# Kernel tuning notes

Measured on AMD Instinct MI355X. Metric: run time of the kernel, lower is better.

## Reference

```python
import jax, jax.numpy as jnp
import numpy as np

N = 100000      # nodes
E = 1600000     # edges
NINP = 64       # input node features
NE = 8          # edge attr channels (spectral supports)
NOUT = 24       # nout1 == nout2
NIN = 2 * NOUT  # 48, hidden width after concat
G = 256         # graphs in batch
EPS = 1e-5


def setup_inputs() -> dict:
    key = jax.random.key(0)
    ks = jax.random.split(key, 40)
    def nrm(i, shape, s=1.0):
        return jax.random.normal(ks[i], shape, dtype=jnp.float32) * s
    inp = {}
    inp["x"] = nrm(0, (N, NINP))
    inp["edge_index"] = jax.random.randint(ks[1], (2, E), 0, N)
    inp["edge_attr"] = nrm(2, (E, NE))
    inp["batch"] = jnp.sort(jax.random.randint(ks[3], (N,), 0, G))
    i = 4
    for l, din in ((1, NINP), (2, NIN), (3, NIN)):
        inp[f"W{l}"] = nrm(i, (NE, din, NOUT), 0.1); i += 1   # SpectConv weight [K,in,out]
        inp[f"b{l}"] = jnp.zeros((NOUT,), jnp.float32)         # SpectConv bias
        inp[f"A{l}"] = nrm(i, (din, NOUT), 0.1); i += 1        # fc11 weight
        inp[f"a{l}"] = jnp.zeros((NOUT,), jnp.float32)
        inp[f"B{l}"] = nrm(i, (din, NOUT), 0.1); i += 1        # fc12 weight
        inp[f"c{l}"] = jnp.zeros((NOUT,), jnp.float32)
        inp[f"g{l}"] = jnp.ones((NIN,), jnp.float32)           # BN gamma
        inp[f"be{l}"] = jnp.zeros((NIN,), jnp.float32)         # BN beta
    inp["F1"] = nrm(i, (NIN, 32), 0.1); i += 1
    inp["f1"] = jnp.zeros((32,), jnp.float32)
    inp["F2"] = nrm(i, (32, 1), 0.1); i += 1
    inp["f2"] = jnp.zeros((1,), jnp.float32)
    return inp


def _ml3(x, src, dst, ea, W, b, A, a, Bm, c):
    # SpectConv (selfconn=False): sum_k segment_sum(ea[:,k]*x[src] -> dst) @ W[k] + b
    xs = x[src]                                    # [E, F] gather
    acc = jnp.zeros((x.shape[0], W.shape[2]), x.dtype)
    for k in range(W.shape[0]):                    # small fixed K=NE loop
        h = jax.ops.segment_sum(ea[:, k:k+1] * xs, dst, num_segments=x.shape[0])
        acc = acc + h @ W[k]
    conv = jax.nn.relu(acc + b)
    gate = jax.nn.relu(x @ A + a) * jnp.tanh(x @ Bm + c)
    return jnp.concatenate([conv, gate], axis=1)   # [N, NIN]


def _bn(x, g, b):
    # BatchNorm1d, training mode (biased batch statistics)
    m = x.mean(0)
    v = x.var(0)
    return (x - m) * jax.lax.rsqrt(v + EPS) * g + b


def reference(x, edge_index, edge_attr, batch,
              W1, b1, A1, a1, B1, c1, g1, be1,
              W2, b2, A2, a2, B2, c2, g2, be2,
              W3, b3, A3, a3, B3, c3, g3, be3,
              F1, f1, F2, f2):
    src, dst = edge_index[0], edge_index[1]
    h = _bn(_ml3(x, src, dst, edge_attr, W1, b1, A1, a1, B1, c1), g1, be1)
    h = _bn(_ml3(h, src, dst, edge_attr, W2, b2, A2, a2, B2, c2), g2, be2)
    h = _bn(_ml3(h, src, dst, edge_attr, W3, b3, A3, a3, B3, c3), g3, be3)
    sums = jax.ops.segment_sum(h, batch, num_segments=G)
    cnts = jax.ops.segment_sum(jnp.ones((h.shape[0], 1), h.dtype), batch, num_segments=G)
    pooled = sums / jnp.maximum(cnts, 1.0)         # global_mean_pool
    return jax.nn.relu(pooled @ F1 + f1) @ F2 + f2  # [G, 1]
```

## Files before the change

### kernel.cpp

```cpp
#include <hip/hip_runtime.h>
#include <hip/hip_fp16.h>
#include <math.h>

#define N_NODES 100000
#define N_EDGES 1600000
#define NGRAPH  256
#define YCOLS   240
#define EPS     1e-5f
#define BNCHUNK 100

typedef _Float16 h2v  __attribute__((ext_vector_type(2)));
typedef _Float16 f16x8 __attribute__((ext_vector_type(8)));
typedef float    f32x4 __attribute__((ext_vector_type(4)));

#if defined(__has_builtin)
#if __has_builtin(__builtin_amdgcn_fdot2)
#define HAVE_FDOT2 1
#endif
#endif

__device__ inline float dot8(float4 yraw, float4 eraw, float acc) {
#ifdef HAVE_FDOT2
  union U { float4 f; h2v v[4]; } y, e;
  y.f = yraw; e.f = eraw;
  acc = __builtin_amdgcn_fdot2(y.v[0], e.v[0], acc, false);
  acc = __builtin_amdgcn_fdot2(y.v[1], e.v[1], acc, false);
  acc = __builtin_amdgcn_fdot2(y.v[2], e.v[2], acc, false);
  acc = __builtin_amdgcn_fdot2(y.v[3], e.v[3], acc, false);
#else
  const __half2* yh = reinterpret_cast<const __half2*>(&yraw);
  const __half2* eh = reinterpret_cast<const __half2*>(&eraw);
#pragma unroll
  for (int i = 0; i < 4; i++) {
    float2 a = __half22float2(yh[i]), b = __half22float2(eh[i]);
    acc += a.x * b.x + a.y * b.y;
  }
#endif
  return acc;
}

__global__ void k_count(const int* __restrict__ dst, int* __restrict__ deg) {
  int e = blockIdx.x * blockDim.x + threadIdx.x;
  if (e < N_EDGES) atomicAdd(&deg[dst[e]], 1);
}

__global__ void k_scan1(const int* __restrict__ deg, int* __restrict__ part,
                        int* __restrict__ bsum) {
  __shared__ int lds[256];
  int t = threadIdx.x;
  int base = blockIdx.x * 1024 + t * 4;
  int v[4]; int s = 0;
#pragma unroll
  for (int i = 0; i < 4; i++) { int idx = base + i; v[i] = (idx < N_NODES) ? deg[idx] : 0; s += v[i]; }
  lds[t] = s; __syncthreads();
  for (int off = 1; off < 256; off <<= 1) {
    int x = (t >= off) ? lds[t - off] : 0;
    __syncthreads();
    lds[t] += x;
    __syncthreads();
  }
  int excl = lds[t] - s;
#pragma unroll
  for (int i = 0; i < 4; i++) { int idx = base + i; if (idx < N_NODES) part[idx] = excl; excl += v[i]; }
  if (t == 255) bsum[blockIdx.x] = lds[255];
}

__global__ void k_scan2(int* __restrict__ bsum, int nb) {
  __shared__ int lds[128];
  int t = threadIdx.x;
  int v = (t < nb) ? bsum[t] : 0;
  lds[t] = v; __syncthreads();
  for (int off = 1; off < 128; off <<= 1) {
    int x = (t >= off) ? lds[t - off] : 0;
    __syncthreads();
    lds[t] += x;
    __syncthreads();
  }
  if (t < nb) bsum[t] = lds[t] - v;
}

__global__ void k_scan3(int* __restrict__ rowptr, const int* __restrict__ bsum,
                        int* __restrict__ cursor) {
  int i = blockIdx.x * blockDim.x + threadIdx.x;
  if (i < N_NODES) {
    int v = rowptr[i] + bsum[i >> 10];
    rowptr[i] = v; cursor[i] = v;
  }
  if (i == 0) rowptr[N_NODES] = N_EDGES;
}

__global__ void k_fill(const int* __restrict__ src, const int* __restrict__ dst,
                       const float* __restrict__ ea, int* __restrict__ cursor,
                       int* __restrict__ esrc, __half* __restrict__ ea_csr) {
  int e = blockIdx.x * blockDim.x + threadIdx.x;
  if (e < N_EDGES) {
    int d = dst[e];
    int pos = atomicAdd(&cursor[d], 1);
    esrc[pos] = src[e];
    float4 a = *reinterpret_cast<const float4*>(ea + (size_t)e * 8);
    float4 b = *reinterpret_cast<const float4*>(ea + (size_t)e * 8 + 4);
    union { __half h[8]; float4 f; } u;
    u.h[0] = __float2half(a.x); u.h[1] = __float2half(a.y);
    u.h[2] = __float2half(a.z); u.h[3] = __float2half(a.w);
    u.h[4] = __float2half(b.x); u.h[5] = __float2half(b.y);
    u.h[6] = __float2half(b.z); u.h[7] = __float2half(b.w);
    *reinterpret_cast<float4*>(ea_csr + (size_t)pos * 8) = u.f;
  }
}

__global__ void k_ghist(const int* __restrict__ batch, int* __restrict__ gcnt) {
  __shared__ int lh[NGRAPH];
  int t = threadIdx.x;
  lh[t] = 0; __syncthreads();
  for (int i = blockIdx.x * 256 + t; i < N_NODES; i += gridDim.x * 256)
    atomicAdd(&lh[batch[i]], 1);
  __syncthreads();
  if (lh[t]) atomicAdd(&gcnt[t], lh[t]);
}

__global__ void k_gscan(const int* __restrict__ gcnt, int* __restrict__ gstart) {
  __shared__ int lds[NGRAPH];
  int t = threadIdx.x;
  int v = gcnt[t]; lds[t] = v; __syncthreads();
  for (int off = 1; off < NGRAPH; off <<= 1) {
    int x = (t >= off) ? lds[t - off] : 0;
    __syncthreads();
    lds[t] += x;
    __syncthreads();
  }
  gstart[t] = lds[t] - v;
  if (t == NGRAPH - 1) gstart[NGRAPH] = lds[NGRAPH - 1];
}

__global__ void k_wcat_h(const float* __restrict__ W, const float* __restrict__ A,
                         const float* __restrict__ B, __half* __restrict__ out,
                         int din) {
  int i = blockIdx.x * blockDim.x + threadIdx.x;
  if (i >= YCOLS * 64) return;
  int j = i / 64, f = i % 64;
  float v = 0.f;
  if (f < din) {
    if (j < 192)      { int k8 = j / 24, o = j - k8 * 24; v = W[(k8 * din + f) * 24 + o]; }
    else if (j < 216) v = A[f * 24 + (j - 192)];
    else              v = B[f * 24 + (j - 216)];
  }
  out[i] = __float2half(v);
}

template <int F>
__global__ __launch_bounds__(256) void k_mm(const float* __restrict__ X,
                                            const __half* __restrict__ Wct,
                                            const float* __restrict__ ss,
                                            __half* __restrict__ Yh,
                                            float* __restrict__ G) {
  __shared__ _Float16 sx[64][64];
  int t = threadIdx.x;
  int r0 = blockIdx.x * 64;
  constexpr int F4 = F / 4;
  for (int i = t; i < 64 * F4; i += 256) {
    int row = i / F4, c4 = i - row * F4;
    int grow = r0 + row;
    float4 v = make_float4(0.f, 0.f, 0.f, 0.f);
    if (grow < N_NODES) {
      v = *reinterpret_cast<const float4*>(X + (size_t)grow * F + c4 * 4);
      if (ss) {
        int f = c4 * 4;
        v.x = v.x * ss[f + 0] + ss[48 + f + 0];
        v.y = v.y * ss[f + 1] + ss[48 + f + 1];
        v.z = v.z * ss[f + 2] + ss[48 + f + 2];
        v.w = v.w * ss[f + 3] + ss[48 + f + 3];
      }
    }
    int c = c4 * 4;
    sx[row][c + 0] = (_Float16)v.x;
    sx[row][c + 1] = (_Float16)v.y;
    sx[row][c + 2] = (_Float16)v.z;
    sx[row][c + 3] = (_Float16)v.w;
  }
  if (F == 48) {
    for (int i = t; i < 64 * 16; i += 256) {
      int row = i / 16, k = 48 + (i - (i / 16) * 16);
      sx[row][k] = (_Float16)0.f;
    }
  }
  __syncthreads();

  int w = t >> 6, l = t & 63;
  int lrow = l & 15;
  int lk = (l >> 4) * 8;
  const f16x8 a0 = *reinterpret_cast<const f16x8*>(&sx[w * 16 + lrow][lk]);
  const f16x8 a1 = *reinterpret_cast<const f16x8*>(&sx[w * 16 + lrow][lk + 32]);
  const _Float16* wct = reinterpret_cast<const _Float16*>(Wct);

#pragma unroll
  for (int ct = 0; ct < 15; ct++) {
    int col = ct * 16 + lrow;
    f16x8 b0 = *reinterpret_cast<const f16x8*>(wct + col * 64 + lk);
    f16x8 b1 = *reinterpret_cast<const f16x8*>(wct + col * 64 + lk + 32);
    f32x4 acc = {0.f, 0.f, 0.f, 0.f};
    acc = __builtin_amdgcn_mfma_f32_16x16x32_f16(a0, b0, acc, 0, 0, 0);
    acc = __builtin_amdgcn_mfma_f32_16x16x32_f16(a1, b1, acc, 0, 0, 0);
    int ycol = (col % 24) * 8 + col / 24;
    int gc   = (col < 216) ? (col - 192) : (24 + col - 216);
#pragma unroll
    for (int r = 0; r < 4; r++) {
      int grow = r0 + w * 16 + (l >> 4) * 4 + r;
      if (grow < N_NODES) {
        if (col < 192) Yh[(size_t)grow * 192 + ycol] = __float2half(acc[r]);
        else           G[(size_t)grow * 48 + gc] = acc[r];
      }
    }
  }
}

__global__ __launch_bounds__(192) void k_agg(
    const __half* __restrict__ Yh, const float* __restrict__ G,
    const int* __restrict__ rowptr, const int* __restrict__ esrc,
    const __half* __restrict__ ea_csr,
    const float* __restrict__ bconv, const float* __restrict__ ba,
    const float* __restrict__ bc,
    float* __restrict__ h, float* __restrict__ partial) {
  __shared__ float ssum[48], ssq[48];
  __shared__ float lacc[2][4][24];
  int t = threadIdx.x;
  if (t < 48) { ssum[t] = 0.f; ssq[t] = 0.f; }
  int ln   = t / 96;
  int slot = (t / 24) % 4;
  int o    = t % 24;
  int n = blockIdx.x * 2 + ln;
  float acc = 0.f;
  if (n < N_NODES) {
    int r0 = rowptr[n], r1 = rowptr[n + 1];
    int idx = r0 + slot;
    for (; idx + 4 < r1; idx += 8) {
      int s0 = esrc[idx], s1 = esrc[idx + 4];
      float4 e0 = *reinterpret_cast<const float4*>(ea_csr + (size_t)idx * 8);
      float4 e1 = *reinterpret_cast<const float4*>(ea_csr + (size_t)(idx + 4) * 8);
      float4 y0 = *reinterpret_cast<const float4*>(Yh + (size_t)s0 * 192 + o * 8);
      float4 y1 = *reinterpret_cast<const float4*>(Yh + (size_t)s1 * 192 + o * 8);
      acc = dot8(y0, e0, acc);
      acc = dot8(y1, e1, acc);
    }
    if (idx < r1) {
      int s0 = esrc[idx];
      float4 e0 = *reinterpret_cast<const float4*>(ea_csr + (size_t)idx * 8);
      float4 y0 = *reinterpret_cast<const float4*>(Yh + (size_t)s0 * 192 + o * 8);
      acc = dot8(y0, e0, acc);
    }
  }
  lacc[ln][slot][o] = acc;
  __syncthreads();
  if (t < 48) {
    int ln2 = t / 24, oo = t % 24;
    int n2 = blockIdx.x * 2 + ln2;
    if (n2 < N_NODES) {
      float a = lacc[ln2][0][oo] + lacc[ln2][1][oo] + lacc[ln2][2][oo] + lacc[ln2][3][oo];
      float conv = fmaxf(a + bconv[oo], 0.f);
      const float* gr = &G[(size_t)n2 * 48];
      float gate = fmaxf(gr[oo] + ba[oo], 0.f) * tanhf(gr[24 + oo] + bc[oo]);
      float* hr = &h[(size_t)n2 * 48];
      hr[oo] = conv;
      hr[24 + oo] = gate;
      atomicAdd(&ssum[oo], conv);        atomicAdd(&ssq[oo], conv * conv);
      atomicAdd(&ssum[24 + oo], gate);   atomicAdd(&ssq[24 + oo], gate * gate);
    }
  }
  __syncthreads();
  if (t < 96) partial[(size_t)blockIdx.x * 96 + t] = (t < 48) ? ssum[t] : ssq[t - 48];
}

__global__ __launch_bounds__(192) void k_bnred1(const float* __restrict__ partial,
                                                int nrows,
                                                float* __restrict__ out) {
  __shared__ float lds[192];
  int t = threadIdx.x;
  int rp = t / 96;
  int c  = t % 96;
  int r0 = blockIdx.x * BNCHUNK;
  int r1 = r0 + BNCHUNK; if (r1 > nrows) r1 = nrows;
  float s = 0.f;
  for (int r = r0 + rp; r < r1; r += 2) s += partial[(size_t)r * 96 + c];
  lds[t] = s; __syncthreads();
  if (t < 96) out[(size_t)blockIdx.x * 96 + t] = lds[t] + lds[t + 96];
}

__global__ void k_bnstats(const float* __restrict__ partial, int nblk,
                          const float* __restrict__ g, const float* __restrict__ be,
                          float* __restrict__ ss) {
  __shared__ float ls[256], lq[256];
  int c = blockIdx.x, t = threadIdx.x;
  float s = 0.f, q = 0.f;
  for (int i = t; i < nblk; i += 256) { s += partial[(size_t)i * 96 + c]; q += partial[(size_t)i * 96 + 48 + c]; }
  ls[t] = s; lq[t] = q; __syncthreads();
  for (int off = 128; off > 0; off >>= 1) {
    if (t < off) { ls[t] += ls[t + off]; lq[t] += lq[t + off]; }
    __syncthreads();
  }
  if (t == 0) {
    float mean = ls[0] / (float)N_NODES;
    float var = lq[0] / (float)N_NODES - mean * mean;
    var = fmaxf(var, 0.f);
    float sc = g[c] * rsqrtf(var + EPS);
    ss[c] = sc;
    ss[48 + c] = be[c] - mean * sc;
  }
}

__global__ __launch_bounds__(240) void k_pool2(const float* __restrict__ h,
                                               const int* __restrict__ gstart,
                                               const float* __restrict__ ss,
                                               float* __restrict__ pooled) {
  __shared__ float acc[240];
  int g = blockIdx.x, t = threadIdx.x;
  int o = t % 48, r = t / 48;
  int n0 = gstart[g], n1 = gstart[g + 1];
  float s = 0.f;
  for (int n = n0 + r; n < n1; n += 5) s += h[(size_t)n * 48 + o];
  acc[t] = s; __syncthreads();
  if (t < 48) {
    float tot = acc[t] + acc[t + 48] + acc[t + 96] + acc[t + 144] + acc[t + 192];
    float cnt = (float)(n1 - n0);
    float mean = tot / fmaxf(cnt, 1.f);
    pooled[g * 48 + t] = mean * ss[t] + ss[48 + t];
  }
}

__global__ __launch_bounds__(64) void k_mlp(const float* __restrict__ pooled,
                                            const float* __restrict__ F1,
                                            const float* __restrict__ f1,
                                            const float* __restrict__ F2,
                                            const float* __restrict__ f2,
                                            float* __restrict__ out) {
  __shared__ float p[48];
  int g = blockIdx.x, t = threadIdx.x;
  if (t < 48) p[t] = pooled[g * 48 + t];
  __syncthreads();
  float r = 0.f;
  if (t < 32) {
    float s = f1[t];
#pragma unroll
    for (int c = 0; c < 48; c++) s += p[c] * F1[c * 32 + t];
    r = fmaxf(s, 0.f) * F2[t];
  }
  for (int off = 32; off > 0; off >>= 1) r += __shfl_down(r, off, 64);
  if (t == 0) out[g] = r + f2[0];
}

extern "C" void kernel_launch(void* const* d_in, const int* in_sizes, int n_in,
                              void* d_out, int out_size, void* d_ws, size_t ws_size,
                              hipStream_t stream) {
  const float* x          = (const float*)d_in[0];
  const int*   edge_index = (const int*)d_in[1];
  const float* ea         = (const float*)d_in[2];
  const int*   batch      = (const int*)d_in[3];
  const float *W[3], *bcv[3], *A[3], *ba[3], *B[3], *bc[3], *g[3], *be[3];
  for (int l = 0; l < 3; l++) {
    int base = 4 + l * 8;
    W[l]   = (const float*)d_in[base + 0];
    bcv[l] = (const float*)d_in[base + 1];
    A[l]   = (const float*)d_in[base + 2];
    ba[l]  = (const float*)d_in[base + 3];
    B[l]   = (const float*)d_in[base + 4];
    bc[l]  = (const float*)d_in[base + 5];
    g[l]   = (const float*)d_in[base + 6];
    be[l]  = (const float*)d_in[base + 7];
  }
  const float* F1 = (const float*)d_in[28];
  const float* f1 = (const float*)d_in[29];
  const float* F2 = (const float*)d_in[30];
  const float* f2 = (const float*)d_in[31];
  const int* src = edge_index;
  const int* dst = edge_index + N_EDGES;

  char* w = (char*)d_ws;
  auto alloc = [&](size_t bytes) -> char* {
    char* p = w;
    w += (bytes + 255) & ~(size_t)255;
    return p;
  };
  int nagg = (N_NODES + 1) / 2;
  int nred = (nagg + BNCHUNK - 1) / BNCHUNK;

  int*    rowptr  = (int*)alloc((N_NODES + 1) * 4);
  int*    cursor  = (int*)alloc((size_t)N_NODES * 4);
  int*    deg     = (int*)alloc((size_t)N_NODES * 4);
  int*    bsum    = (int*)alloc(128 * 4);
  int*    esrc    = (int*)alloc((size_t)N_EDGES * 4);
  __half* ea_csr  = (__half*)alloc((size_t)N_EDGES * 8 * 2);
  int*    gcnt    = (int*)alloc(NGRAPH * 4);
  int*    gstart  = (int*)alloc((NGRAPH + 1) * 4);
  __half* Wct1    = (__half*)alloc((size_t)YCOLS * 64 * 2);
  __half* Wct2    = (__half*)alloc((size_t)YCOLS * 64 * 2);
  __half* Wct3    = (__half*)alloc((size_t)YCOLS * 64 * 2);
  __half* Yh      = (__half*)alloc((size_t)N_NODES * 192 * 2);
  float*  G       = (float*)alloc((size_t)N_NODES * 48 * 4);
  float*  h       = (float*)alloc((size_t)N_NODES * 48 * 4);
  float*  partial = (float*)alloc((size_t)nagg * 96 * 4);
  float*  partial2= (float*)alloc((size_t)nred * 96 * 4);
  float*  ss1     = (float*)alloc(96 * 4);
  float*  ss2     = (float*)alloc(96 * 4);
  float*  ss3     = (float*)alloc(96 * 4);
  float*  pooled  = (float*)alloc(NGRAPH * 48 * 4);

  hipMemsetAsync(deg, 0, (size_t)N_NODES * 4, stream);
  hipMemsetAsync(gcnt, 0, NGRAPH * 4, stream);

  k_count<<<(N_EDGES + 255) / 256, 256, 0, stream>>>(dst, deg);
  int nchunk = (N_NODES + 1023) / 1024;
  k_scan1<<<nchunk, 256, 0, stream>>>(deg, rowptr, bsum);
  k_scan2<<<1, 128, 0, stream>>>(bsum, nchunk);
  k_scan3<<<(N_NODES + 255) / 256, 256, 0, stream>>>(rowptr, bsum, cursor);
  k_fill<<<(N_EDGES + 255) / 256, 256, 0, stream>>>(src, dst, ea, cursor, esrc, ea_csr);

  k_ghist<<<64, 256, 0, stream>>>(batch, gcnt);
  k_gscan<<<1, NGRAPH, 0, stream>>>(gcnt, gstart);

  k_wcat_h<<<(YCOLS * 64 + 255) / 256, 256, 0, stream>>>(W[0], A[0], B[0], Wct1, 64);
  k_wcat_h<<<(YCOLS * 64 + 255) / 256, 256, 0, stream>>>(W[1], A[1], B[1], Wct2, 48);
  k_wcat_h<<<(YCOLS * 64 + 255) / 256, 256, 0, stream>>>(W[2], A[2], B[2], Wct3, 48);

  int nmm = (N_NODES + 63) / 64;

  k_mm<64><<<nmm, 256, 0, stream>>>(x, Wct1, nullptr, Yh, G);
  k_agg<<<nagg, 192, 0, stream>>>(Yh, G, rowptr, esrc, ea_csr, bcv[0], ba[0], bc[0], h, partial);
  k_bnred1<<<nred, 192, 0, stream>>>(partial, nagg, partial2);
  k_bnstats<<<48, 256, 0, stream>>>(partial2, nred, g[0], be[0], ss1);
  k_mm<48><<<nmm, 256, 0, stream>>>(h, Wct2, ss1, Yh, G);
  k_agg<<<nagg, 192, 0, stream>>>(Yh, G, rowptr, esrc, ea_csr, bcv[1], ba[1], bc[1], h, partial);
  k_bnred1<<<nred, 192, 0, stream>>>(partial, nagg, partial2);
  k_bnstats<<<48, 256, 0, stream>>>(partial2, nred, g[1], be[1], ss2);
  k_mm<48><<<nmm, 256, 0, stream>>>(h, Wct3, ss2, Yh, G);
  k_agg<<<nagg, 192, 0, stream>>>(Yh, G, rowptr, esrc, ea_csr, bcv[2], ba[2], bc[2], h, partial);
  k_bnred1<<<nred, 192, 0, stream>>>(partial, nagg, partial2);
  k_bnstats<<<48, 256, 0, stream>>>(partial2, nred, g[2], be[2], ss3);

  k_pool2<<<NGRAPH, 240, 0, stream>>>(h, gstart, ss3, pooled);
  k_mlp<<<NGRAPH, 64, 0, stream>>>(pooled, F1, f1, F2, f2, (float*)d_out);
}
```

Baseline: 707.7 us.

## Degree-sort nodes for aggregation, widen agg blocks, split CSR fill

Nodes are bucketed by in-degree through a counting sort (histogram, scan, fill) and the aggregation kernel visits them in that order, so the nodes sharing a block have similar work. The aggregation block grows to 768 threads, covering 4 nodes with 8 edge slots each, which gives more parallelism per node. The CSR fill is split into an atomic pass that records edge ids and a second pass that gathers src and edge attributes and writes them contiguously. The costs are extra small kernels and an indirect perm lookup in aggregation, and node writes to h become scattered.

```diff
diff --git a/kernel.cpp b/kernel.cpp
--- a/kernel.cpp
+++ b/kernel.cpp
@@ -8,6 +8,7 @@
 #define YCOLS   240
 #define EPS     1e-5f
 #define BNCHUNK 100
+#define DEGB    64
 
 typedef _Float16 h2v  __attribute__((ext_vector_type(2)));
 typedef _Float16 f16x8 __attribute__((ext_vector_type(8)));
@@ -89,14 +90,22 @@
   if (i == 0) rowptr[N_NODES] = N_EDGES;
 }
 
-__global__ void k_fill(const int* __restrict__ src, const int* __restrict__ dst,
-                       const float* __restrict__ ea, int* __restrict__ cursor,
-                       int* __restrict__ esrc, __half* __restrict__ ea_csr) {
+__global__ void k_fillA(const int* __restrict__ dst, int* __restrict__ cursor,
+                        int* __restrict__ eidx) {
   int e = blockIdx.x * blockDim.x + threadIdx.x;
   if (e < N_EDGES) {
-    int d = dst[e];
-    int pos = atomicAdd(&cursor[d], 1);
-    esrc[pos] = src[e];
+    int pos = atomicAdd(&cursor[dst[e]], 1);
+    eidx[pos] = e;
+  }
+}
+
+__global__ void k_fillB(const int* __restrict__ eidx, const int* __restrict__ src,
+                        const float* __restrict__ ea,
+                        int* __restrict__ esrc, __half* __restrict__ ea_csr) {
+  int p = blockIdx.x * blockDim.x + threadIdx.x;
+  if (p < N_EDGES) {
+    int e = eidx[p];
+    esrc[p] = src[e];
     float4 a = *reinterpret_cast<const float4*>(ea + (size_t)e * 8);
     float4 b = *reinterpret_cast<const float4*>(ea + (size_t)e * 8 + 4);
     union { __half h[8]; float4 f; } u;
@@ -104,7 +113,38 @@
     u.h[2] = __float2half(a.z); u.h[3] = __float2half(a.w);
     u.h[4] = __float2half(b.x); u.h[5] = __float2half(b.y);
     u.h[6] = __float2half(b.z); u.h[7] = __float2half(b.w);
-    *reinterpret_cast<float4*>(ea_csr + (size_t)pos * 8) = u.f;
+    *reinterpret_cast<float4*>(ea_csr + (size_t)p * 8) = u.f;
+  }
+}
+
+__global__ void k_dhist(const int* __restrict__ deg, int* __restrict__ dhist) {
+  int n = blockIdx.x * blockDim.x + threadIdx.x;
+  if (n < N_NODES) {
+    int d = deg[n]; if (d > DEGB - 1) d = DEGB - 1;
+    atomicAdd(&dhist[d], 1);
+  }
+}
+
+__global__ void k_dscan(const int* __restrict__ dhist, int* __restrict__ dcur) {
+  __shared__ int lds[DEGB];
+  int t = threadIdx.x;
+  int v = dhist[t]; lds[t] = v; __syncthreads();
+  for (int off = 1; off < DEGB; off <<= 1) {
+    int x = (t >= off) ? lds[t - off] : 0;
+    __syncthreads();
+    lds[t] += x;
+    __syncthreads();
+  }
+  dcur[t] = lds[t] - v;
+}
+
+__global__ void k_dfill(const int* __restrict__ deg, int* __restrict__ dcur,
+                        int* __restrict__ perm) {
+  int n = blockIdx.x * blockDim.x + threadIdx.x;
+  if (n < N_NODES) {
+    int d = deg[n]; if (d > DEGB - 1) d = DEGB - 1;
+    int pos = atomicAdd(&dcur[d], 1);
+    perm[pos] = n;
   }
 }
 
@@ -213,29 +253,30 @@
   }
 }
 
-__global__ __launch_bounds__(192) void k_agg(
+__global__ __launch_bounds__(768) void k_agg(
     const __half* __restrict__ Yh, const float* __restrict__ G,
-    const int* __restrict__ rowptr, const int* __restrict__ esrc,
-    const __half* __restrict__ ea_csr,
+    const int* __restrict__ rowptr, const int* __restrict__ perm,
+    const int* __restrict__ esrc, const __half* __restrict__ ea_csr,
     const float* __restrict__ bconv, const float* __restrict__ ba,
     const float* __restrict__ bc,
     float* __restrict__ h, float* __restrict__ partial) {
   __shared__ float ssum[48], ssq[48];
-  __shared__ float lacc[2][4][24];
+  __shared__ float lacc[4][8][24];
   int t = threadIdx.x;
   if (t < 48) { ssum[t] = 0.f; ssq[t] = 0.f; }
-  int ln   = t / 96;
-  int slot = (t / 24) % 4;
+  int ln   = t / 192;
+  int slot = (t / 24) % 8;
   int o    = t % 24;
-  int n = blockIdx.x * 2 + ln;
+  int bi = blockIdx.x * 4 + ln;
   float acc = 0.f;
-  if (n < N_NODES) {
+  if (bi < N_NODES) {
+    int n = perm[bi];
     int r0 = rowptr[n], r1 = rowptr[n + 1];
     int idx = r0 + slot;
-    for (; idx + 4 < r1; idx += 8) {
-      int s0 = esrc[idx], s1 = esrc[idx + 4];
+    for (; idx + 8 < r1; idx += 16) {
+      int s0 = esrc[idx], s1 = esrc[idx + 8];
       float4 e0 = *reinterpret_cast<const float4*>(ea_csr + (size_t)idx * 8);
-      float4 e1 = *reinterpret_cast<const float4*>(ea_csr + (size_t)(idx + 4) * 8);
+      float4 e1 = *reinterpret_cast<const float4*>(ea_csr + (size_t)(idx + 8) * 8);
       float4 y0 = *reinterpret_cast<const float4*>(Yh + (size_t)s0 * 192 + o * 8);
       float4 y1 = *reinterpret_cast<const float4*>(Yh + (size_t)s1 * 192 + o * 8);
       acc = dot8(y0, e0, acc);
@@ -250,11 +291,14 @@
   }
   lacc[ln][slot][o] = acc;
   __syncthreads();
-  if (t < 48) {
+  if (t < 96) {
     int ln2 = t / 24, oo = t % 24;
-    int n2 = blockIdx.x * 2 + ln2;
-    if (n2 < N_NODES) {
-      float a = lacc[ln2][0][oo] + lacc[ln2][1][oo] + lacc[ln2][2][oo] + lacc[ln2][3][oo];
+    int bi2 = blockIdx.x * 4 + ln2;
+    if (bi2 < N_NODES) {
+      int n2 = perm[bi2];
+      float a = 0.f;
+#pragma unroll
+      for (int s = 0; s < 8; s++) a += lacc[ln2][s][oo];
       float conv = fmaxf(a + bconv[oo], 0.f);
       const float* gr = &G[(size_t)n2 * 48];
       float gate = fmaxf(gr[oo] + ba[oo], 0.f) * tanhf(gr[24 + oo] + bc[oo]);
@@ -378,15 +422,19 @@
     w += (bytes + 255) & ~(size_t)255;
     return p;
   };
-  int nagg = (N_NODES + 1) / 2;
+  int nagg = (N_NODES + 3) / 4;
   int nred = (nagg + BNCHUNK - 1) / BNCHUNK;
 
   int*    rowptr  = (int*)alloc((N_NODES + 1) * 4);
   int*    cursor  = (int*)alloc((size_t)N_NODES * 4);
   int*    deg     = (int*)alloc((size_t)N_NODES * 4);
   int*    bsum    = (int*)alloc(128 * 4);
+  int*    eidx    = (int*)alloc((size_t)N_EDGES * 4);
   int*    esrc    = (int*)alloc((size_t)N_EDGES * 4);
   __half* ea_csr  = (__half*)alloc((size_t)N_EDGES * 8 * 2);
+  int*    perm    = (int*)alloc((size_t)N_NODES * 4);
+  int*    dhist   = (int*)alloc(DEGB * 4);
+  int*    dcur    = (int*)alloc(DEGB * 4);
   int*    gcnt    = (int*)alloc(NGRAPH * 4);
   int*    gstart  = (int*)alloc((NGRAPH + 1) * 4);
   __half* Wct1    = (__half*)alloc((size_t)YCOLS * 64 * 2);
@@ -404,13 +452,19 @@
 
   hipMemsetAsync(deg, 0, (size_t)N_NODES * 4, stream);
   hipMemsetAsync(gcnt, 0, NGRAPH * 4, stream);
+  hipMemsetAsync(dhist, 0, DEGB * 4, stream);
 
   k_count<<<(N_EDGES + 255) / 256, 256, 0, stream>>>(dst, deg);
   int nchunk = (N_NODES + 1023) / 1024;
   k_scan1<<<nchunk, 256, 0, stream>>>(deg, rowptr, bsum);
   k_scan2<<<1, 128, 0, stream>>>(bsum, nchunk);
   k_scan3<<<(N_NODES + 255) / 256, 256, 0, stream>>>(rowptr, bsum, cursor);
-  k_fill<<<(N_EDGES + 255) / 256, 256, 0, stream>>>(src, dst, ea, cursor, esrc, ea_csr);
+  k_fillA<<<(N_EDGES + 255) / 256, 256, 0, stream>>>(dst, cursor, eidx);
+  k_fillB<<<(N_EDGES + 255) / 256, 256, 0, stream>>>(eidx, src, ea, esrc, ea_csr);
+
+  k_dhist<<<(N_NODES + 255) / 256, 256, 0, stream>>>(deg, dhist);
+  k_dscan<<<1, DEGB, 0, stream>>>(dhist, dcur);
+  k_dfill<<<(N_NODES + 255) / 256, 256, 0, stream>>>(deg, dcur, perm);
 
   k_ghist<<<64, 256, 0, stream>>>(batch, gcnt);
   k_gscan<<<1, NGRAPH, 0, stream>>>(gcnt, gstart);
@@ -422,15 +476,15 @@
   int nmm = (N_NODES + 63) / 64;
 
   k_mm<64><<<nmm, 256, 0, stream>>>(x, Wct1, nullptr, Yh, G);
-  k_agg<<<nagg, 192, 0, stream>>>(Yh, G, rowptr, esrc, ea_csr, bcv[0], ba[0], bc[0], h, partial);
+  k_agg<<<nagg, 768, 0, stream>>>(Yh, G, rowptr, perm, esrc, ea_csr, bcv[0], ba[0], bc[0], h, partial);
   k_bnred1<<<nred, 192, 0, stream>>>(partial, nagg, partial2);
   k_bnstats<<<48, 256, 0, stream>>>(partial2, nred, g[0], be[0], ss1);
   k_mm<48><<<nmm, 256, 0, stream>>>(h, Wct2, ss1, Yh, G);
-  k_agg<<<nagg, 192, 0, stream>>>(Yh, G, rowptr, esrc, ea_csr, bcv[1], ba[1], bc[1], h, partial);
+  k_agg<<<nagg, 768, 0, stream>>>(Yh, G, rowptr, perm, esrc, ea_csr, bcv[1], ba[1], bc[1], h, partial);
   k_bnred1<<<nred, 192, 0, stream>>>(partial, nagg, partial2);
   k_bnstats<<<48, 256, 0, stream>>>(partial2, nred, g[1], be[1], ss2);
   k_mm<48><<<nmm, 256, 0, stream>>>(h, Wct3, ss2, Yh, G);
-  k_agg<<<nagg, 192, 0, stream>>>(Yh, G, rowptr, esrc, ea_csr, bcv[2], ba[2], bc[2], h, partial);
+  k_agg<<<nagg, 768, 0, stream>>>(Yh, G, rowptr, perm, esrc, ea_csr, bcv[2], ba[2], bc[2], h, partial);
   k_bnred1<<<nred, 192, 0, stream>>>(partial, nagg, partial2);
   k_bnstats<<<48, 256, 0, stream>>>(partial2, nred, g[2], be[2], ss3);
 
```

Result: slower. 1.586 ms (+124.1%).

## Fuse gate into matmul epilogue, stage outputs in LDS, move BN stats to separate pass

Applied to the files above, without the earlier changes.

The matmul kernel now stages its MFMA outputs in shared memory and writes Yh with coalesced vector stores. It also computes the gated branch (relu*tanh) directly into h, which removes the G intermediate buffer. The aggregation kernel only writes the conv half, with its edge loop unrolled to four edges per slot. Batch-norm sums are now computed by a separate reduction pass over h instead of LDS atomics, and ping-pong h buffers avoid read/write aliasing. This trades an extra read of h for less global traffic on G and fewer scattered stores.

```diff
diff --git a/kernel.cpp b/kernel.cpp
--- a/kernel.cpp
+++ b/kernel.cpp
@@ -7,7 +7,7 @@
 #define NGRAPH  256
 #define YCOLS   240
 #define EPS     1e-5f
-#define BNCHUNK 100
+#define BNCHUNK 200
 
 typedef _Float16 h2v  __attribute__((ext_vector_type(2)));
 typedef _Float16 f16x8 __attribute__((ext_vector_type(8)));
@@ -151,9 +151,13 @@
 __global__ __launch_bounds__(256) void k_mm(const float* __restrict__ X,
                                             const __half* __restrict__ Wct,
                                             const float* __restrict__ ss,
+                                            const float* __restrict__ ba,
+                                            const float* __restrict__ bc,
                                             __half* __restrict__ Yh,
-                                            float* __restrict__ G) {
+                                            float* __restrict__ h) {
   __shared__ _Float16 sx[64][64];
+  __shared__ _Float16 sy[64][200];
+  __shared__ float    sg[64][52];
   int t = threadIdx.x;
   int r0 = blockIdx.x * 64;
   constexpr int F4 = F / 4;
@@ -179,7 +183,7 @@
   }
   if (F == 48) {
     for (int i = t; i < 64 * 16; i += 256) {
-      int row = i / 16, k = 48 + (i - (i / 16) * 16);
+      int row = i / 16, k = 48 + (i % 16);
       sx[row][k] = (_Float16)0.f;
     }
   }
@@ -204,26 +208,32 @@
     int gc   = (col < 216) ? (col - 192) : (24 + col - 216);
 #pragma unroll
     for (int r = 0; r < 4; r++) {
-      int grow = r0 + w * 16 + (l >> 4) * 4 + r;
-      if (grow < N_NODES) {
-        if (col < 192) Yh[(size_t)grow * 192 + ycol] = __float2half(acc[r]);
-        else           G[(size_t)grow * 48 + gc] = acc[r];
-      }
-    }
+      int row = w * 16 + (l >> 4) * 4 + r;
+      if (col < 192) sy[row][ycol] = (_Float16)acc[r];
+      else           sg[row][gc] = acc[r];
+    }
+  }
+  __syncthreads();
+
+  int rows = N_NODES - r0; if (rows > 64) rows = 64;
+  for (int i = t; i < rows * 48; i += 256) {
+    int row = i / 48, c = (i % 48) * 4;
+    *reinterpret_cast<uint2*>(Yh + (size_t)(r0 + row) * 192 + c) =
+        *reinterpret_cast<const uint2*>(&sy[row][c]);
+  }
+  for (int i = t; i < rows * 24; i += 256) {
+    int row = i / 24, o = i % 24;
+    float gate = fmaxf(sg[row][o] + ba[o], 0.f) * tanhf(sg[row][24 + o] + bc[o]);
+    h[(size_t)(r0 + row) * 48 + 24 + o] = gate;
   }
 }
 
 __global__ __launch_bounds__(192) void k_agg(
-    const __half* __restrict__ Yh, const float* __restrict__ G,
-    const int* __restrict__ rowptr, const int* __restrict__ esrc,
-    const __half* __restrict__ ea_csr,
-    const float* __restrict__ bconv, const float* __restrict__ ba,
-    const float* __restrict__ bc,
-    float* __restrict__ h, float* __restrict__ partial) {
-  __shared__ float ssum[48], ssq[48];
+    const __half* __restrict__ Yh, const int* __restrict__ rowptr,
+    const int* __restrict__ esrc, const __half* __restrict__ ea_csr,
+    const float* __restrict__ bconv, float* __restrict__ h) {
   __shared__ float lacc[2][4][24];
   int t = threadIdx.x;
-  if (t < 48) { ssum[t] = 0.f; ssq[t] = 0.f; }
   int ln   = t / 96;
   int slot = (t / 24) % 4;
   int o    = t % 24;
@@ -232,16 +242,22 @@
   if (n < N_NODES) {
     int r0 = rowptr[n], r1 = rowptr[n + 1];
     int idx = r0 + slot;
-    for (; idx + 4 < r1; idx += 8) {
-      int s0 = esrc[idx], s1 = esrc[idx + 4];
+    for (; idx + 12 < r1; idx += 16) {
+      int s0 = esrc[idx], s1 = esrc[idx + 4], s2 = esrc[idx + 8], s3 = esrc[idx + 12];
       float4 e0 = *reinterpret_cast<const float4*>(ea_csr + (size_t)idx * 8);
       float4 e1 = *reinterpret_cast<const float4*>(ea_csr + (size_t)(idx + 4) * 8);
+      float4 e2 = *reinterpret_cast<const float4*>(ea_csr + (size_t)(idx + 8) * 8);
+      float4 e3 = *reinterpret_cast<const float4*>(ea_csr + (size_t)(idx + 12) * 8);
       float4 y0 = *reinterpret_cast<const float4*>(Yh + (size_t)s0 * 192 + o * 8);
       float4 y1 = *reinterpret_cast<const float4*>(Yh + (size_t)s1 * 192 + o * 8);
+      float4 y2 = *reinterpret_cast<const float4*>(Yh + (size_t)s2 * 192 + o * 8);
+      float4 y3 = *reinterpret_cast<const float4*>(Yh + (size_t)s3 * 192 + o * 8);
       acc = dot8(y0, e0, acc);
       acc = dot8(y1, e1, acc);
-    }
-    if (idx < r1) {
+      acc = dot8(y2, e2, acc);
+      acc = dot8(y3, e3, acc);
+    }
+    for (; idx < r1; idx += 4) {
       int s0 = esrc[idx];
       float4 e0 = *reinterpret_cast<const float4*>(ea_csr + (size_t)idx * 8);
       float4 y0 = *reinterpret_cast<const float4*>(Yh + (size_t)s0 * 192 + o * 8);
@@ -255,33 +271,30 @@
     int n2 = blockIdx.x * 2 + ln2;
     if (n2 < N_NODES) {
       float a = lacc[ln2][0][oo] + lacc[ln2][1][oo] + lacc[ln2][2][oo] + lacc[ln2][3][oo];
-      float conv = fmaxf(a + bconv[oo], 0.f);
-      const float* gr = &G[(size_t)n2 * 48];
-      float gate = fmaxf(gr[oo] + ba[oo], 0.f) * tanhf(gr[24 + oo] + bc[oo]);
-      float* hr = &h[(size_t)n2 * 48];
-      hr[oo] = conv;
-      hr[24 + oo] = gate;
-      atomicAdd(&ssum[oo], conv);        atomicAdd(&ssq[oo], conv * conv);
-      atomicAdd(&ssum[24 + oo], gate);   atomicAdd(&ssq[24 + oo], gate * gate);
-    }
-  }
-  __syncthreads();
-  if (t < 96) partial[(size_t)blockIdx.x * 96 + t] = (t < 48) ? ssum[t] : ssq[t - 48];
-}
-
-__global__ __launch_bounds__(192) void k_bnred1(const float* __restrict__ partial,
-                                                int nrows,
+      h[(size_t)n2 * 48 + oo] = fmaxf(a + bconv[oo], 0.f);
+    }
+  }
+}
+
+__global__ __launch_bounds__(192) void k_bnred1(const float* __restrict__ h,
                                                 float* __restrict__ out) {
-  __shared__ float lds[192];
-  int t = threadIdx.x;
-  int rp = t / 96;
-  int c  = t % 96;
+  __shared__ float lsum[192], lsq[192];
+  int t = threadIdx.x;
+  int rp = t / 48, c = t % 48;
   int r0 = blockIdx.x * BNCHUNK;
-  int r1 = r0 + BNCHUNK; if (r1 > nrows) r1 = nrows;
-  float s = 0.f;
-  for (int r = r0 + rp; r < r1; r += 2) s += partial[(size_t)r * 96 + c];
-  lds[t] = s; __syncthreads();
-  if (t < 96) out[(size_t)blockIdx.x * 96 + t] = lds[t] + lds[t + 96];
+  int r1 = r0 + BNCHUNK; if (r1 > N_NODES) r1 = N_NODES;
+  float s = 0.f, q = 0.f;
+  for (int r = r0 + rp; r < r1; r += 4) {
+    float v = h[(size_t)r * 48 + c];
+    s += v; q += v * v;
+  }
+  lsum[t] = s; lsq[t] = q; __syncthreads();
+  if (t < 48) {
+    float S = lsum[t] + lsum[t + 48] + lsum[t + 96] + lsum[t + 144];
+    float Q = lsq[t] + lsq[t + 48] + lsq[t + 96] + lsq[t + 144];
+    out[(size_t)blockIdx.x * 96 + t] = S;
+    out[(size_t)blockIdx.x * 96 + 48 + t] = Q;
+  }
 }
 
 __global__ void k_bnstats(const float* __restrict__ partial, int nblk,
@@ -379,7 +392,7 @@
     return p;
   };
   int nagg = (N_NODES + 1) / 2;
-  int nred = (nagg + BNCHUNK - 1) / BNCHUNK;
+  int nred = (N_NODES + BNCHUNK - 1) / BNCHUNK;
 
   int*    rowptr  = (int*)alloc((N_NODES + 1) * 4);
   int*    cursor  = (int*)alloc((size_t)N_NODES * 4);
@@ -393,9 +406,8 @@
   __half* Wct2    = (__half*)alloc((size_t)YCOLS * 64 * 2);
   __half* Wct3    = (__half*)alloc((size_t)YCOLS * 64 * 2);
   __half* Yh      = (__half*)alloc((size_t)N_NODES * 192 * 2);
-  float*  G       = (float*)alloc((size_t)N_NODES * 48 * 4);
-  float*  h       = (float*)alloc((size_t)N_NODES * 48 * 4);
-  float*  partial = (float*)alloc((size_t)nagg * 96 * 4);
+  float*  h0      = (float*)alloc((size_t)N_NODES * 48 * 4);
+  float*  h1      = (float*)alloc((size_t)N_NODES * 48 * 4);
   float*  partial2= (float*)alloc((size_t)nred * 96 * 4);
   float*  ss1     = (float*)alloc(96 * 4);
   float*  ss2     = (float*)alloc(96 * 4);
@@ -421,19 +433,19 @@
 
   int nmm = (N_NODES + 63) / 64;
 
-  k_mm<64><<<nmm, 256, 0, stream>>>(x, Wct1, nullptr, Yh, G);
-  k_agg<<<nagg, 192, 0, stream>>>(Yh, G, rowptr, esrc, ea_csr, bcv[0], ba[0], bc[0], h, partial);
-  k_bnred1<<<nred, 192, 0, stream>>>(partial, nagg, partial2);
+  k_mm<64><<<nmm, 256, 0, stream>>>(x, Wct1, nullptr, ba[0], bc[0], Yh, h0);
+  k_agg<<<nagg, 192, 0, stream>>>(Yh, rowptr, esrc, ea_csr, bcv[0], h0);
+  k_bnred1<<<nred, 192, 0, stream>>>(h0, partial2);
   k_bnstats<<<48, 256, 0, stream>>>(partial2, nred, g[0], be[0], ss1);
-  k_mm<48><<<nmm, 256, 0, stream>>>(h, Wct2, ss1, Yh, G);
-  k_agg<<<nagg, 192, 0, stream>>>(Yh, G, rowptr, esrc, ea_csr, bcv[1], ba[1], bc[1], h, partial);
-  k_bnred1<<<nred, 192, 0, stream>>>(partial, nagg, partial2);
+  k_mm<48><<<nmm, 256, 0, stream>>>(h0, Wct2, ss1, ba[1], bc[1], Yh, h1);
+  k_agg<<<nagg, 192, 0, stream>>>(Yh, rowptr, esrc, ea_csr, bcv[1], h1);
+  k_bnred1<<<nred, 192, 0, stream>>>(h1, partial2);
   k_bnstats<<<48, 256, 0, stream>>>(partial2, nred, g[1], be[1], ss2);
-  k_mm<48><<<nmm, 256, 0, stream>>>(h, Wct3, ss2, Yh, G);
-  k_agg<<<nagg, 192, 0, stream>>>(Yh, G, rowptr, esrc, ea_csr, bcv[2], ba[2], bc[2], h, partial);
-  k_bnred1<<<nred, 192, 0, stream>>>(partial, nagg, partial2);
+  k_mm<48><<<nmm, 256, 0, stream>>>(h1, Wct3, ss2, ba[2], bc[2], Yh, h0);
+  k_agg<<<nagg, 192, 0, stream>>>(Yh, rowptr, esrc, ea_csr, bcv[2], h0);
+  k_bnred1<<<nred, 192, 0, stream>>>(h0, partial2);
   k_bnstats<<<48, 256, 0, stream>>>(partial2, nred, g[2], be[2], ss3);
 
-  k_pool2<<<NGRAPH, 240, 0, stream>>>(h, gstart, ss3, pooled);
+  k_pool2<<<NGRAPH, 240, 0, stream>>>(h0, gstart, ss3, pooled);
   k_mlp<<<NGRAPH, 64, 0, stream>>>(pooled, F1, f1, F2, f2, (float*)d_out);
 }
```

New measurement: 645.8 us. 1.1x faster.
